# Kernel tuning notes

Hardware: AMD Instinct MI355X
Metric: run time of the kernel (lower is better)

Reference implementation:

```python
import jax, jax.numpy as jnp
import numpy as np

B, C, H, W, N = 16, 81, 128, 128, 64


def setup_inputs() -> dict:
    key = jax.random.key(0)
    k1, k2, k3, k4, k5 = jax.random.split(key, 5)
    bbox_pred = jax.random.normal(k1, (B, 4, H, W), jnp.float32)
    class_pred = jax.random.normal(k2, (B, C, H, W), jnp.float32)
    # well-formed GT boxes in [0,1]: x1y1 + positive wh
    xy = jax.random.uniform(k3, (B, N, 2), jnp.float32)
    wh = jax.random.uniform(k4, (B, N, 2), jnp.float32) * 0.5 + 0.05
    boxes = jnp.concatenate([xy, xy + wh], axis=-1)  # [B,N,4]
    labels = jax.random.randint(k5, (B, N), 0, C).astype(jnp.int32)
    return {"bbox_pred": bbox_pred, "class_pred": class_pred,
            "boxes": boxes, "labels": labels}


def reference(bbox_pred, class_pred, boxes, labels):
    Bb, Cc, Hh, Ww = class_pred.shape
    A = Hh * Ww
    pb = bbox_pred.transpose(0, 2, 3, 1).reshape(Bb, A, 4)   # [B,A,4]
    pc = class_pred.transpose(0, 2, 3, 1).reshape(Bb, A, Cc)  # [B,A,C]

    # pairwise IoU [B,A,N] via broadcasting (pred [B,A,1,4] vs gt [B,1,N,4])
    p = pb[:, :, None, :]
    g = boxes[:, None, :, :]
    ix1 = jnp.maximum(p[..., 0], g[..., 0])
    iy1 = jnp.maximum(p[..., 1], g[..., 1])
    ix2 = jnp.minimum(p[..., 2], g[..., 2])
    iy2 = jnp.minimum(p[..., 3], g[..., 3])
    inter = jnp.clip(ix2 - ix1, 0) * jnp.clip(iy2 - iy1, 0)
    pa = (pb[..., 2] - pb[..., 0]) * (pb[..., 3] - pb[..., 1])      # [B,A]
    ga = (boxes[..., 2] - boxes[..., 0]) * (boxes[..., 3] - boxes[..., 1])  # [B,N]
    union = pa[:, :, None] + ga[:, None, :] - inter
    ious = inter / union

    max_ious = ious.max(axis=-1)            # [B,A]
    max_idx = jnp.argmax(ious, axis=-1)     # [B,A]
    pos = max_ious > 0.5                    # [B,A]
    posf = pos.astype(pc.dtype)
    npos = posf.sum(axis=-1)                # [B]
    denom = jnp.maximum(npos, 1.0)

    assigned_labels = jnp.take_along_axis(labels, max_idx, axis=1)          # [B,A]
    assigned_boxes = jnp.take_along_axis(boxes, max_idx[..., None], axis=1)  # [B,A,4]

    # cross-entropy per anchor (mean over positives)
    logp = jax.nn.log_softmax(pc, axis=-1)
    ce = -jnp.take_along_axis(logp, assigned_labels[..., None], axis=2)[..., 0]
    cls_loss = (ce * posf).sum(axis=-1) / denom

    # smooth-L1 (beta=1), mean over positive elements (npos*4)
    diff = pb - assigned_boxes
    ad = jnp.abs(diff)
    sl1 = jnp.where(ad < 1.0, 0.5 * diff * diff, ad - 0.5)
    reg_loss = (sl1 * posf[..., None]).sum(axis=(-1, -2)) / (denom * 4.0)

    # fallback when an image has zero positives: CE with all-zero labels
    zero_loss = -logp[..., 0].mean(axis=-1)

    per_img = jnp.where(npos > 0, cls_loss + reg_loss, zero_loss)
    return per_img.mean()
```

## Files before the change

### kernel.cpp

```cpp
#include <hip/hip_runtime.h>
#include <math.h>

#define Bc 16
#define Cc 81
#define AA 16384
#define Nn 64
#define TPB 256
#define BLOCKS_PER_IMG (AA / TPB)
#define NBLOCKS (Bc * BLOCKS_PER_IMG)
#define G 9
#define NG 9

__global__ __launch_bounds__(TPB) void det_loss_main(
    const float* __restrict__ bbox_pred,
    const float* __restrict__ class_pred,
    const float* __restrict__ boxes,
    const int* __restrict__ labels,
    float4* __restrict__ ws_part)
{
    __shared__ float4 sbox[Nn];
    __shared__ float  sga[Nn];
    __shared__ int    slab[Nn];

    const int blk  = blockIdx.x;
    const int b    = blk / BLOCKS_PER_IMG;
    const int ablk = blk % BLOCKS_PER_IMG;
    const int t    = threadIdx.x;

    if (t < Nn) {
        float4 g = ((const float4*)boxes)[b * Nn + t];
        sbox[t] = g;
        sga[t]  = (g.z - g.x) * (g.w - g.y);
        slab[t] = labels[b * Nn + t];
    }
    __syncthreads();

    const int a = ablk * TPB + t;

    const float* bp = bbox_pred + (size_t)b * 4 * AA + a;
    const float px1 = bp[0 * AA];
    const float py1 = bp[1 * AA];
    const float px2 = bp[2 * AA];
    const float py2 = bp[3 * AA];
    const float pa  = (px2 - px1) * (py2 - py1);

    const float* cp = class_pred + (size_t)b * Cc * AA + a;
    float buf0[G], buf1[G];
#pragma unroll
    for (int k = 0; k < G; ++k) buf0[k] = cp[(size_t)k * AA];

    float best = -INFINITY;
    int   bj   = 0;
#pragma unroll 8
    for (int j = 0; j < Nn; ++j) {
        const float4 g  = sbox[j];
        const float ix1 = fmaxf(px1, g.x);
        const float iy1 = fmaxf(py1, g.y);
        const float ix2 = fminf(px2, g.z);
        const float iy2 = fminf(py2, g.w);
        const float inter = fmaxf(ix2 - ix1, 0.0f) * fmaxf(iy2 - iy1, 0.0f);
        const float iou = inter * __builtin_amdgcn_rcpf(pa + sga[j] - inter);
        if (iou > best) { best = iou; bj = j; }
    }
    const float posf = (best > 0.5f) ? 1.0f : 0.0f;
    const int    lab = slab[bj];
    const float4 gb  = sbox[bj];

    float sA = 0.0f, sB = 0.0f, x0 = 0.0f, xl = 0.0f;
#pragma unroll
    for (int g = 0; g < NG; ++g) {
        if (g + 1 < NG) {
            if ((g & 1) == 0) {
#pragma unroll
                for (int k = 0; k < G; ++k)
                    buf1[k] = cp[(size_t)((g + 1) * G + k) * AA];
            } else {
#pragma unroll
                for (int k = 0; k < G; ++k)
                    buf0[k] = cp[(size_t)((g + 1) * G + k) * AA];
            }
        }
#pragma unroll
        for (int k = 0; k < G; ++k) {
            const float x = ((g & 1) == 0) ? buf0[k] : buf1[k];
            const int   c = g * G + k;
            if (c == 0) x0 = x;
            xl = (c == lab) ? x : xl;
            if (k & 1) sB += __expf(x);
            else       sA += __expf(x);
        }
    }
    const float lse   = __logf(sA + sB);
    const float ce    = (lse - xl) * posf;
    const float logp0 = x0 - lse;

    float sl = 0.0f;
    {
        const float d0 = px1 - gb.x, d1 = py1 - gb.y, d2 = px2 - gb.z, d3 = py2 - gb.w;
        const float a0 = fabsf(d0), a1 = fabsf(d1), a2 = fabsf(d2), a3 = fabsf(d3);
        sl += (a0 < 1.0f) ? 0.5f * d0 * d0 : a0 - 0.5f;
        sl += (a1 < 1.0f) ? 0.5f * d1 * d1 : a1 - 0.5f;
        sl += (a2 < 1.0f) ? 0.5f * d2 * d2 : a2 - 0.5f;
        sl += (a3 < 1.0f) ? 0.5f * d3 * d3 : a3 - 0.5f;
        sl *= posf;
    }

    float v0 = posf, v1 = ce, v2 = sl, v3 = logp0;
#pragma unroll
    for (int o = 32; o > 0; o >>= 1) {
        v0 += __shfl_down(v0, o);
        v1 += __shfl_down(v1, o);
        v2 += __shfl_down(v2, o);
        v3 += __shfl_down(v3, o);
    }
    __shared__ float4 red[4];
    const int wave = t >> 6, lane = t & 63;
    if (lane == 0) red[wave] = make_float4(v0, v1, v2, v3);
    __syncthreads();
    if (t == 0) {
        float4 r0 = red[0], r1 = red[1], r2 = red[2], r3 = red[3];
        ws_part[blk] = make_float4(r0.x + r1.x + r2.x + r3.x,
                                   r0.y + r1.y + r2.y + r3.y,
                                   r0.z + r1.z + r2.z + r3.z,
                                   r0.w + r1.w + r2.w + r3.w);
    }
}

__global__ __launch_bounds__(256) void det_loss_final(
    const float4* __restrict__ ws_part, float* __restrict__ out)
{
    const int t = threadIdx.x;
    float4 p0 = ws_part[t];
    float4 p1 = ws_part[t + 256];
    float4 p2 = ws_part[t + 512];
    float4 p3 = ws_part[t + 768];
#pragma unroll
    for (int o = 1; o < 64; o <<= 1) {
        p0.x += __shfl_xor(p0.x, o); p0.y += __shfl_xor(p0.y, o);
        p0.z += __shfl_xor(p0.z, o); p0.w += __shfl_xor(p0.w, o);
        p1.x += __shfl_xor(p1.x, o); p1.y += __shfl_xor(p1.y, o);
        p1.z += __shfl_xor(p1.z, o); p1.w += __shfl_xor(p1.w, o);
        p2.x += __shfl_xor(p2.x, o); p2.y += __shfl_xor(p2.y, o);
        p2.z += __shfl_xor(p2.z, o); p2.w += __shfl_xor(p2.w, o);
        p3.x += __shfl_xor(p3.x, o); p3.y += __shfl_xor(p3.y, o);
        p3.z += __shfl_xor(p3.z, o); p3.w += __shfl_xor(p3.w, o);
    }
    __shared__ float4 simg[16];
    const int lane = t & 63, w = t >> 6;
    if (lane == 0) {
        simg[w]      = p0;
        simg[w + 4]  = p1;
        simg[w + 8]  = p2;
        simg[w + 12] = p3;
    }
    __syncthreads();
    float per = 0.0f;
    if (t < Bc) {
        const float4 s = simg[t];
        const float npos = s.x;
        const float denom = fmaxf(npos, 1.0f);
        const float cls_reg = s.y / denom + s.z / (denom * 4.0f);
        const float zero_loss = -s.w / (float)AA;
        per = (npos > 0.0f) ? cls_reg : zero_loss;
    }
#pragma unroll
    for (int o = 8; o > 0; o >>= 1) per += __shfl_down(per, o);
    if (t == 0) out[0] = per * (1.0f / (float)Bc);
}

extern "C" void kernel_launch(void* const* d_in, const int* in_sizes, int n_in,
                              void* d_out, int out_size, void* d_ws, size_t ws_size,
                              hipStream_t stream) {
    const float* bbox_pred  = (const float*)d_in[0];
    const float* class_pred = (const float*)d_in[1];
    const float* boxes      = (const float*)d_in[2];
    const int*   labels     = (const int*)d_in[3];
    float* out = (float*)d_out;
    float4* ws = (float4*)d_ws;

    det_loss_main<<<NBLOCKS, TPB, 0, stream>>>(bbox_pred, class_pred, boxes, labels, ws);
    det_loss_final<<<1, 256, 0, stream>>>(ws, out);
}
```

Measured before the change: 24.49 us.

## Split class channels across waves with float4 anchor loads and LDS combine

Changes the class-logit load from one scalar per anchor per channel to each wave reading a contiguous float4 of four anchors for an interleaved subset of channels (w, w+4, ...). Partial exp-sums, label logits and the channel-0 logit are written to LDS and summed per anchor after a barrier. The goal is wider 16-byte global loads and fewer load instructions per thread on this memory-bound stream. The cost is two extra barriers, more LDS traffic, and a label broadcast through LDS.

```diff
diff --git a/kernel.cpp b/kernel.cpp
--- a/kernel.cpp
+++ b/kernel.cpp
@@ -6,10 +6,9 @@
 #define AA 16384
 #define Nn 64
 #define TPB 256
-#define BLOCKS_PER_IMG (AA / TPB)
+#define ABLK 256
+#define BLOCKS_PER_IMG (AA / ABLK)
 #define NBLOCKS (Bc * BLOCKS_PER_IMG)
-#define G 9
-#define NG 9
 
 __global__ __launch_bounds__(TPB) void det_loss_main(
     const float* __restrict__ bbox_pred,
@@ -18,14 +17,21 @@
     const int* __restrict__ labels,
     float4* __restrict__ ws_part)
 {
-    __shared__ float4 sbox[Nn];
-    __shared__ float  sga[Nn];
-    __shared__ int    slab[Nn];
+    __shared__ __align__(16) float4 sbox[Nn];
+    __shared__ float sga[Nn];
+    __shared__ int   slab[Nn];
+    __shared__ __align__(16) int   lab_lds[ABLK];
+    __shared__ __align__(16) float s_sum[4][ABLK];
+    __shared__ __align__(16) float s_xl[4][ABLK];
+    __shared__ __align__(16) float s_x0[ABLK];
 
     const int blk  = blockIdx.x;
     const int b    = blk / BLOCKS_PER_IMG;
     const int ablk = blk % BLOCKS_PER_IMG;
     const int t    = threadIdx.x;
+    const int w    = t >> 6;
+    const int l    = t & 63;
+    const int base = ablk * ABLK;
 
     if (t < Nn) {
         float4 g = ((const float4*)boxes)[b * Nn + t];
@@ -33,21 +39,21 @@
         sga[t]  = (g.z - g.x) * (g.w - g.y);
         slab[t] = labels[b * Nn + t];
     }
-    __syncthreads();
-
-    const int a = ablk * TPB + t;
-
-    const float* bp = bbox_pred + (size_t)b * 4 * AA + a;
+
+    const float* bp = bbox_pred + (size_t)b * 4 * AA + base + t;
     const float px1 = bp[0 * AA];
     const float py1 = bp[1 * AA];
     const float px2 = bp[2 * AA];
     const float py2 = bp[3 * AA];
     const float pa  = (px2 - px1) * (py2 - py1);
 
-    const float* cp = class_pred + (size_t)b * Cc * AA + a;
-    float buf0[G], buf1[G];
-#pragma unroll
-    for (int k = 0; k < G; ++k) buf0[k] = cp[(size_t)k * AA];
+    __syncthreads();
+
+    const float* cpw = class_pred + (size_t)b * Cc * AA + base + 4 * l;
+    const int nk = (w == 0) ? 21 : 20;
+    float4 buf0 = *(const float4*)(cpw + (size_t)(w + 0) * AA);
+    float4 buf1 = *(const float4*)(cpw + (size_t)(w + 4) * AA);
+    float4 buf2 = *(const float4*)(cpw + (size_t)(w + 8) * AA);
 
     float best = -INFINITY;
     int   bj   = 0;
@@ -66,33 +72,46 @@
     const int    lab = slab[bj];
     const float4 gb  = sbox[bj];
 
-    float sA = 0.0f, sB = 0.0f, x0 = 0.0f, xl = 0.0f;
-#pragma unroll
-    for (int g = 0; g < NG; ++g) {
-        if (g + 1 < NG) {
-            if ((g & 1) == 0) {
-#pragma unroll
-                for (int k = 0; k < G; ++k)
-                    buf1[k] = cp[(size_t)((g + 1) * G + k) * AA];
-            } else {
-#pragma unroll
-                for (int k = 0; k < G; ++k)
-                    buf0[k] = cp[(size_t)((g + 1) * G + k) * AA];
+    lab_lds[t] = lab;
+    __syncthreads();
+
+    const int4 labv = ((const int4*)lab_lds)[l];
+
+    float s0 = 0.0f, s1 = 0.0f, s2 = 0.0f, s3 = 0.0f;
+    float y0 = 0.0f, y1 = 0.0f, y2 = 0.0f, y3 = 0.0f;
+    float4 x0v = make_float4(0.0f, 0.0f, 0.0f, 0.0f);
+#pragma unroll
+    for (int k = 0; k < 21; ++k) {
+        if (k < nk) {
+            const int m = k % 3;
+            const float4 x = (m == 0) ? buf0 : ((m == 1) ? buf1 : buf2);
+            if (k + 3 < nk) {
+                const float4 nx = *(const float4*)(cpw + (size_t)(w + 4 * (k + 3)) * AA);
+                if (m == 0) buf0 = nx; else if (m == 1) buf1 = nx; else buf2 = nx;
             }
+            const int c = w + 4 * k;
+            if (k == 0) { if (w == 0) x0v = x; }
+            y0 += (c == labv.x) ? x.x : 0.0f;
+            y1 += (c == labv.y) ? x.y : 0.0f;
+            y2 += (c == labv.z) ? x.z : 0.0f;
+            y3 += (c == labv.w) ? x.w : 0.0f;
+            s0 += __expf(x.x);
+            s1 += __expf(x.y);
+            s2 += __expf(x.z);
+            s3 += __expf(x.w);
         }
-#pragma unroll
-        for (int k = 0; k < G; ++k) {
-            const float x = ((g & 1) == 0) ? buf0[k] : buf1[k];
-            const int   c = g * G + k;
-            if (c == 0) x0 = x;
-            xl = (c == lab) ? x : xl;
-            if (k & 1) sB += __expf(x);
-            else       sA += __expf(x);
-        }
-    }
-    const float lse   = __logf(sA + sB);
-    const float ce    = (lse - xl) * posf;
-    const float logp0 = x0 - lse;
+    }
+
+    ((float4*)s_sum[w])[l] = make_float4(s0, s1, s2, s3);
+    ((float4*)s_xl[w])[l]  = make_float4(y0, y1, y2, y3);
+    if (w == 0) ((float4*)s_x0)[l] = x0v;
+    __syncthreads();
+
+    const float sumexp = s_sum[0][t] + s_sum[1][t] + s_sum[2][t] + s_sum[3][t];
+    const float xl     = s_xl[0][t]  + s_xl[1][t]  + s_xl[2][t]  + s_xl[3][t];
+    const float lse    = __logf(sumexp);
+    const float ce     = (lse - xl) * posf;
+    const float logp0  = s_x0[t] - lse;
 
     float sl = 0.0f;
     {
@@ -114,8 +133,7 @@
         v3 += __shfl_down(v3, o);
     }
     __shared__ float4 red[4];
-    const int wave = t >> 6, lane = t & 63;
-    if (lane == 0) red[wave] = make_float4(v0, v1, v2, v3);
+    if (l == 0) red[w] = make_float4(v0, v1, v2, v3);
     __syncthreads();
     if (t == 0) {
         float4 r0 = red[0], r1 = red[1], r2 = red[2], r3 = red[3];
```

New measurement: 28.37 us. 1.16x slower.

## Fuse final reduction via last-block atomic counter and triple-buffer class loads

Applied to the files above, without the earlier changes.

Merges the separate final-reduction kernel into the main kernel: each block publishes its partial sums, bumps an atomic counter, and the last block to finish does the cross-block reduction and writes the output. This removes the second kernel launch but adds a memset of the counter, so there are still two stream operations. The class-logit prefetch also moves from double to triple buffering, keeping two groups in flight to hide more memory latency at the cost of more registers.

```diff
diff --git a/kernel.cpp b/kernel.cpp
--- a/kernel.cpp
+++ b/kernel.cpp
@@ -11,16 +11,19 @@
 #define G 9
 #define NG 9
 
-__global__ __launch_bounds__(TPB) void det_loss_main(
+__global__ __launch_bounds__(TPB) void det_loss_fused(
     const float* __restrict__ bbox_pred,
     const float* __restrict__ class_pred,
     const float* __restrict__ boxes,
     const int* __restrict__ labels,
-    float4* __restrict__ ws_part)
+    float4* __restrict__ ws_part,
+    unsigned int* __restrict__ counter,
+    float* __restrict__ out)
 {
     __shared__ float4 sbox[Nn];
     __shared__ float  sga[Nn];
     __shared__ int    slab[Nn];
+    __shared__ int    s_islast;
 
     const int blk  = blockIdx.x;
     const int b    = blk / BLOCKS_PER_IMG;
@@ -45,9 +48,11 @@
     const float pa  = (px2 - px1) * (py2 - py1);
 
     const float* cp = class_pred + (size_t)b * Cc * AA + a;
-    float buf0[G], buf1[G];
+    float buf0[G], buf1[G], buf2[G];
 #pragma unroll
-    for (int k = 0; k < G; ++k) buf0[k] = cp[(size_t)k * AA];
+    for (int k = 0; k < G; ++k) buf0[k] = cp[(size_t)(0 * G + k) * AA];
+#pragma unroll
+    for (int k = 0; k < G; ++k) buf1[k] = cp[(size_t)(1 * G + k) * AA];
 
     float best = -INFINITY;
     int   bj   = 0;
@@ -69,20 +74,23 @@
     float sA = 0.0f, sB = 0.0f, x0 = 0.0f, xl = 0.0f;
 #pragma unroll
     for (int g = 0; g < NG; ++g) {
-        if (g + 1 < NG) {
-            if ((g & 1) == 0) {
+        if (g + 2 < NG) {
+            const int m = (g + 2) % 3;
+            if (m == 0) {
 #pragma unroll
-                for (int k = 0; k < G; ++k)
-                    buf1[k] = cp[(size_t)((g + 1) * G + k) * AA];
+                for (int k = 0; k < G; ++k) buf0[k] = cp[(size_t)((g + 2) * G + k) * AA];
+            } else if (m == 1) {
+#pragma unroll
+                for (int k = 0; k < G; ++k) buf1[k] = cp[(size_t)((g + 2) * G + k) * AA];
             } else {
 #pragma unroll
-                for (int k = 0; k < G; ++k)
-                    buf0[k] = cp[(size_t)((g + 1) * G + k) * AA];
+                for (int k = 0; k < G; ++k) buf2[k] = cp[(size_t)((g + 2) * G + k) * AA];
             }
         }
+        const int mc = g % 3;
 #pragma unroll
         for (int k = 0; k < G; ++k) {
-            const float x = ((g & 1) == 0) ? buf0[k] : buf1[k];
+            const float x = (mc == 0) ? buf0[k] : ((mc == 1) ? buf1[k] : buf2[k]);
             const int   c = g * G + k;
             if (c == 0) x0 = x;
             xl = (c == lab) ? x : xl;
@@ -123,35 +131,37 @@
                                    r0.y + r1.y + r2.y + r3.y,
                                    r0.z + r1.z + r2.z + r3.z,
                                    r0.w + r1.w + r2.w + r3.w);
+        __threadfence();
+        const unsigned int c = atomicAdd(counter, 1u);
+        s_islast = (c == NBLOCKS - 1) ? 1 : 0;
     }
-}
+    __syncthreads();
+    if (!s_islast) return;
 
-__global__ __launch_bounds__(256) void det_loss_final(
-    const float4* __restrict__ ws_part, float* __restrict__ out)
-{
-    const int t = threadIdx.x;
-    float4 p0 = ws_part[t];
-    float4 p1 = ws_part[t + 256];
-    float4 p2 = ws_part[t + 512];
-    float4 p3 = ws_part[t + 768];
+    __threadfence();
+    const float* wsf = (const float*)ws_part;
+    float4 p[4];
+#pragma unroll
+    for (int r = 0; r < 4; ++r) {
+        const float* q = wsf + (size_t)(t + 256 * r) * 4;
+        p[r].x = __hip_atomic_load(q + 0, __ATOMIC_RELAXED, __HIP_MEMORY_SCOPE_AGENT);
+        p[r].y = __hip_atomic_load(q + 1, __ATOMIC_RELAXED, __HIP_MEMORY_SCOPE_AGENT);
+        p[r].z = __hip_atomic_load(q + 2, __ATOMIC_RELAXED, __HIP_MEMORY_SCOPE_AGENT);
+        p[r].w = __hip_atomic_load(q + 3, __ATOMIC_RELAXED, __HIP_MEMORY_SCOPE_AGENT);
+    }
 #pragma unroll
     for (int o = 1; o < 64; o <<= 1) {
-        p0.x += __shfl_xor(p0.x, o); p0.y += __shfl_xor(p0.y, o);
-        p0.z += __shfl_xor(p0.z, o); p0.w += __shfl_xor(p0.w, o);
-        p1.x += __shfl_xor(p1.x, o); p1.y += __shfl_xor(p1.y, o);
-        p1.z += __shfl_xor(p1.z, o); p1.w += __shfl_xor(p1.w, o);
-        p2.x += __shfl_xor(p2.x, o); p2.y += __shfl_xor(p2.y, o);
-        p2.z += __shfl_xor(p2.z, o); p2.w += __shfl_xor(p2.w, o);
-        p3.x += __shfl_xor(p3.x, o); p3.y += __shfl_xor(p3.y, o);
-        p3.z += __shfl_xor(p3.z, o); p3.w += __shfl_xor(p3.w, o);
+#pragma unroll
+        for (int r = 0; r < 4; ++r) {
+            p[r].x += __shfl_xor(p[r].x, o); p[r].y += __shfl_xor(p[r].y, o);
+            p[r].z += __shfl_xor(p[r].z, o); p[r].w += __shfl_xor(p[r].w, o);
+        }
     }
     __shared__ float4 simg[16];
-    const int lane = t & 63, w = t >> 6;
+    const int w2 = t >> 6;
     if (lane == 0) {
-        simg[w]      = p0;
-        simg[w + 4]  = p1;
-        simg[w + 8]  = p2;
-        simg[w + 12] = p3;
+#pragma unroll
+        for (int r = 0; r < 4; ++r) simg[w2 + 4 * r] = p[r];
     }
     __syncthreads();
     float per = 0.0f;
@@ -176,8 +186,10 @@
     const float* boxes      = (const float*)d_in[2];
     const int*   labels     = (const int*)d_in[3];
     float* out = (float*)d_out;
-    float4* ws = (float4*)d_ws;
+    float4* ws_part = (float4*)d_ws;
+    unsigned int* counter = (unsigned int*)((char*)d_ws + (size_t)NBLOCKS * sizeof(float4));
 
-    det_loss_main<<<NBLOCKS, TPB, 0, stream>>>(bbox_pred, class_pred, boxes, labels, ws);
-    det_loss_final<<<1, 256, 0, stream>>>(ws, out);
+    hipMemsetAsync(counter, 0, sizeof(unsigned int), stream);
+    det_loss_fused<<<NBLOCKS, TPB, 0, stream>>>(bbox_pred, class_pred, boxes, labels,
+                                                ws_part, counter, out);
 }
```

After: 54.36 us. 2.22x slower.

## Double block size and triple-buffer class logit loads

Applied to the files above, without the earlier changes.

Raises threads per block from 256 to 512, halving the number of blocks to 512, and adapts the block reduction and the final reduction to the new partial layout (32 partials per image). The class-logit streaming moves from double to triple buffering, prefetching two groups ahead to keep more loads in flight. This raises register pressure and may lower occupancy, in exchange for deeper memory-level parallelism on a bandwidth-bound read of class_pred.

```diff
diff --git a/kernel.cpp b/kernel.cpp
--- a/kernel.cpp
+++ b/kernel.cpp
@@ -5,7 +5,7 @@
 #define Cc 81
 #define AA 16384
 #define Nn 64
-#define TPB 256
+#define TPB 512
 #define BLOCKS_PER_IMG (AA / TPB)
 #define NBLOCKS (Bc * BLOCKS_PER_IMG)
 #define G 9
@@ -45,9 +45,11 @@
     const float pa  = (px2 - px1) * (py2 - py1);
 
     const float* cp = class_pred + (size_t)b * Cc * AA + a;
-    float buf0[G], buf1[G];
+    float buf0[G], buf1[G], buf2[G];
 #pragma unroll
-    for (int k = 0; k < G; ++k) buf0[k] = cp[(size_t)k * AA];
+    for (int k = 0; k < G; ++k) buf0[k] = cp[(size_t)(0 * G + k) * AA];
+#pragma unroll
+    for (int k = 0; k < G; ++k) buf1[k] = cp[(size_t)(1 * G + k) * AA];
 
     float best = -INFINITY;
     int   bj   = 0;
@@ -69,20 +71,23 @@
     float sA = 0.0f, sB = 0.0f, x0 = 0.0f, xl = 0.0f;
 #pragma unroll
     for (int g = 0; g < NG; ++g) {
-        if (g + 1 < NG) {
-            if ((g & 1) == 0) {
+        if (g + 2 < NG) {
+            const int m = (g + 2) % 3;
+            if (m == 0) {
 #pragma unroll
-                for (int k = 0; k < G; ++k)
-                    buf1[k] = cp[(size_t)((g + 1) * G + k) * AA];
+                for (int k = 0; k < G; ++k) buf0[k] = cp[(size_t)((g + 2) * G + k) * AA];
+            } else if (m == 1) {
+#pragma unroll
+                for (int k = 0; k < G; ++k) buf1[k] = cp[(size_t)((g + 2) * G + k) * AA];
             } else {
 #pragma unroll
-                for (int k = 0; k < G; ++k)
-                    buf0[k] = cp[(size_t)((g + 1) * G + k) * AA];
+                for (int k = 0; k < G; ++k) buf2[k] = cp[(size_t)((g + 2) * G + k) * AA];
             }
         }
+        const int mc = g % 3;
 #pragma unroll
         for (int k = 0; k < G; ++k) {
-            const float x = ((g & 1) == 0) ? buf0[k] : buf1[k];
+            const float x = (mc == 0) ? buf0[k] : ((mc == 1) ? buf1[k] : buf2[k]);
             const int   c = g * G + k;
             if (c == 0) x0 = x;
             xl = (c == lab) ? x : xl;
@@ -113,16 +118,17 @@
         v2 += __shfl_down(v2, o);
         v3 += __shfl_down(v3, o);
     }
-    __shared__ float4 red[4];
+    __shared__ float4 red[8];
     const int wave = t >> 6, lane = t & 63;
     if (lane == 0) red[wave] = make_float4(v0, v1, v2, v3);
     __syncthreads();
     if (t == 0) {
-        float4 r0 = red[0], r1 = red[1], r2 = red[2], r3 = red[3];
-        ws_part[blk] = make_float4(r0.x + r1.x + r2.x + r3.x,
-                                   r0.y + r1.y + r2.y + r3.y,
-                                   r0.z + r1.z + r2.z + r3.z,
-                                   r0.w + r1.w + r2.w + r3.w);
+        float4 s = red[0];
+#pragma unroll
+        for (int r = 1; r < 8; ++r) {
+            s.x += red[r].x; s.y += red[r].y; s.z += red[r].z; s.w += red[r].w;
+        }
+        ws_part[blk] = s;
     }
 }
 
@@ -132,26 +138,19 @@
     const int t = threadIdx.x;
     float4 p0 = ws_part[t];
     float4 p1 = ws_part[t + 256];
-    float4 p2 = ws_part[t + 512];
-    float4 p3 = ws_part[t + 768];
 #pragma unroll
-    for (int o = 1; o < 64; o <<= 1) {
+    for (int o = 1; o < 32; o <<= 1) {
         p0.x += __shfl_xor(p0.x, o); p0.y += __shfl_xor(p0.y, o);
         p0.z += __shfl_xor(p0.z, o); p0.w += __shfl_xor(p0.w, o);
         p1.x += __shfl_xor(p1.x, o); p1.y += __shfl_xor(p1.y, o);
         p1.z += __shfl_xor(p1.z, o); p1.w += __shfl_xor(p1.w, o);
-        p2.x += __shfl_xor(p2.x, o); p2.y += __shfl_xor(p2.y, o);
-        p2.z += __shfl_xor(p2.z, o); p2.w += __shfl_xor(p2.w, o);
-        p3.x += __shfl_xor(p3.x, o); p3.y += __shfl_xor(p3.y, o);
-        p3.z += __shfl_xor(p3.z, o); p3.w += __shfl_xor(p3.w, o);
     }
     __shared__ float4 simg[16];
     const int lane = t & 63, w = t >> 6;
-    if (lane == 0) {
-        simg[w]      = p0;
-        simg[w + 4]  = p1;
-        simg[w + 8]  = p2;
-        simg[w + 12] = p3;
+    if (lane == 0 || lane == 32) {
+        const int img = 2 * w + (lane >> 5);
+        simg[img]     = p0;
+        simg[img + 8] = p1;
     }
     __syncthreads();
     float per = 0.0f;
```

Result: no change. 24.03 us (-1.9%).
